# Kernel optimization log

Measured on AMD Instinct MI355X. Metric: run time of the kernel, lower is better.

The kernel has to match this reference:

```python
import jax, jax.numpy as jnp
import numpy as np

N_NODES = 50000
N_EDGES = 600000
F_IN, HID, N_CLS = 128, 128, 40
NEG_SLOPE = 0.2


def _gat_conv(x, src, dst, W, a_src, a_dst, b, num_nodes):
    # x: [N, Fin] -> h: [N, H]  (heads=1 PyG GATConv)
    h = x @ W
    s_src = h @ a_src  # [N]
    s_dst = h @ a_dst  # [N]
    e = jax.nn.leaky_relu(s_src[src] + s_dst[dst], NEG_SLOPE)  # [E]
    # numerically-stable softmax over incoming edges per destination node
    m = jax.ops.segment_max(e, dst, num_segments=num_nodes)  # [N]
    ex = jnp.exp(e - m[dst])
    denom = jax.ops.segment_sum(ex, dst, num_segments=num_nodes)  # [N]
    alpha = ex / denom[dst]  # [E]
    out = jax.ops.segment_sum(alpha[:, None] * h[src], dst, num_segments=num_nodes)
    return out + b


def setup_inputs() -> dict:
    key = jax.random.key(0)
    ks = jax.random.split(key, 10)
    x = jax.random.normal(ks[0], (N_NODES, F_IN), dtype=jnp.float32)
    edge_index = jax.random.randint(ks[1], (2, N_EDGES), 0, N_NODES, dtype=jnp.int64)
    sd = lambda fin: 1.0 / np.sqrt(fin)
    return {
        "x": x,
        "edge_index": edge_index,
        "W1": jax.random.normal(ks[2], (F_IN, HID), dtype=jnp.float32) * sd(F_IN),
        "a1_src": jax.random.normal(ks[3], (HID,), dtype=jnp.float32) * sd(HID),
        "a1_dst": jax.random.normal(ks[4], (HID,), dtype=jnp.float32) * sd(HID),
        "b1": jnp.zeros((HID,), dtype=jnp.float32),
        "W2": jax.random.normal(ks[5], (HID, HID), dtype=jnp.float32) * sd(HID),
        "a2_src": jax.random.normal(ks[6], (HID,), dtype=jnp.float32) * sd(HID),
        "a2_dst": jax.random.normal(ks[7], (HID,), dtype=jnp.float32) * sd(HID),
        "b2": jnp.zeros((HID,), dtype=jnp.float32),
        "Wl": jax.random.normal(ks[8], (HID, N_CLS), dtype=jnp.float32) * sd(HID),
        "bl": jnp.zeros((N_CLS,), dtype=jnp.float32),
    }


def reference(x, edge_index, W1, a1_src, a1_dst, b1, W2, a2_src, a2_dst, b2, Wl, bl):
    n = x.shape[0]
    # PyG GATConv adds self loops by default
    loops = jnp.arange(n, dtype=edge_index.dtype)
    src = jnp.concatenate([edge_index[0], loops])
    dst = jnp.concatenate([edge_index[1], loops])
    h = jax.nn.relu(_gat_conv(x, src, dst, W1, a1_src, a1_dst, b1, n))
    # F.dropout(training=self.training): eval mode -> identity
    h = _gat_conv(h, src, dst, W2, a2_src, a2_dst, b2, n)
    logits = jax.nn.log_softmax(h @ Wl + bl, axis=1)
    return (logits, edge_index)
```

## Files before the change

kernel.cpp:

```cpp
#include <hip/hip_runtime.h>
#include <hip/hip_bf16.h>
#include <math.h>

#define N_NODES 50000
#define N_EDGES 600000
#define TOT_E   (N_EDGES + N_NODES)
#define FDIM    128
#define HROW    64
#define NCLS    40
#define SCAN_B  1024

__device__ inline float bf16_lo(uint32_t u) { return __uint_as_float(u << 16); }
__device__ inline float bf16_hi(uint32_t u) { return __uint_as_float(u & 0xffff0000u); }
__device__ inline uint32_t bf16_pack(float a, float b) {
    uint32_t ua = __float_as_uint(a), ub = __float_as_uint(b);
    uint32_t ra = (ua + 0x7fffu + ((ua >> 16) & 1u)) >> 16;
    uint32_t rb = (ub + 0x7fffu + ((ub >> 16) & 1u)) >> 16;
    return ra | (rb << 16);
}

__global__ void init_counts(int* __restrict__ counts) {
    int i = blockIdx.x * blockDim.x + threadIdx.x;
    if (i < N_NODES) counts[i] = 1;
}

__global__ void hist_kernel(const int* __restrict__ ei, int* __restrict__ counts) {
    int i = blockIdx.x * blockDim.x + threadIdx.x;
    if (i >= N_EDGES / 4) return;
    int4 d = ((const int4*)(ei + N_EDGES))[i];
    atomicAdd(&counts[d.x], 1);
    atomicAdd(&counts[d.y], 1);
    atomicAdd(&counts[d.z], 1);
    atomicAdd(&counts[d.w], 1);
}

__global__ void scan1_kernel(const int* __restrict__ counts, int* __restrict__ excl,
                             int* __restrict__ bsums, int n) {
    __shared__ int ws[16];
    int gid = blockIdx.x * SCAN_B + threadIdx.x;
    int wv = threadIdx.x >> 6, lane = threadIdx.x & 63;
    int v = (gid < n) ? counts[gid] : 0;
    int incl = v;
    #pragma unroll
    for (int off = 1; off < 64; off <<= 1) {
        int t = __shfl_up(incl, off, 64);
        if (lane >= off) incl += t;
    }
    if (lane == 63) ws[wv] = incl;
    __syncthreads();
    int woff = 0;
    for (int i = 0; i < wv; i++) woff += ws[i];
    if (gid < n) excl[gid] = woff + incl - v;
    if (threadIdx.x == SCAN_B - 1) bsums[blockIdx.x] = woff + incl;
}

__global__ void scan3_kernel(int* __restrict__ rowptr, const int* __restrict__ bsums,
                             int* __restrict__ cursor, int n, int total) {
    __shared__ int base_s;
    if (threadIdx.x < 64) {
        int v = (threadIdx.x < (int)blockIdx.x) ? bsums[threadIdx.x] : 0;
        #pragma unroll
        for (int off = 32; off > 0; off >>= 1) v += __shfl_down(v, off, 64);
        if (threadIdx.x == 0) base_s = v;
    }
    __syncthreads();
    int base = base_s;
    int gid = blockIdx.x * SCAN_B + threadIdx.x;
    if (gid < n) {
        int v = rowptr[gid] + base;
        rowptr[gid] = v;
        cursor[gid] = v;
    }
    if (gid == 0) rowptr[n] = total;
}

#define SCAT_T ((N_EDGES / 4) + N_NODES)
__global__ void scatter_kernel(const int* __restrict__ ei, int* __restrict__ cursor,
                               int* __restrict__ adj) {
    int i = blockIdx.x * blockDim.x + threadIdx.x;
    if (i >= SCAT_T) return;
    if (i < N_EDGES / 4) {
        int4 s4 = ((const int4*)ei)[i];
        int4 d4 = ((const int4*)(ei + N_EDGES))[i];
        adj[atomicAdd(&cursor[d4.x], 1)] = s4.x;
        adj[atomicAdd(&cursor[d4.y], 1)] = s4.y;
        adj[atomicAdd(&cursor[d4.z], 1)] = s4.z;
        adj[atomicAdd(&cursor[d4.w], 1)] = s4.w;
    } else {
        int nd = i - N_EDGES / 4;
        adj[atomicAdd(&cursor[nd], 1)] = nd;
    }
}

__global__ void prep_wa(const float* __restrict__ W1, const float* __restrict__ a1s,
                        const float* __restrict__ a1d, const float* __restrict__ W2,
                        const float* __restrict__ a2s, const float* __restrict__ a2d,
                        float* __restrict__ wa) {
    int t = threadIdx.x;
    int vec = t >> 7, k = t & 127;
    const float* W = (vec < 2) ? W1 : W2;
    const float* a = (vec == 0) ? a1s : (vec == 1) ? a1d : (vec == 2) ? a2s : a2d;
    float s = 0.f;
    #pragma unroll 4
    for (int j = 0; j < FDIM; j += 4) {
        float4 wv = *(const float4*)&W[k * FDIM + j];
        float4 av = *(const float4*)&a[j];
        s += wv.x * av.x + wv.y * av.y + wv.z * av.z + wv.w * av.w;
    }
    wa[vec * FDIM + k] = s;
}

#define GR 16
template <bool BF16IN>
__global__ __launch_bounds__(128) void gemm_att_kernel(
        const void* __restrict__ Xin, const float* __restrict__ W,
        const float* __restrict__ wa_s, const float* __restrict__ wa_d,
        uint32_t* __restrict__ H, float* __restrict__ ssrc, float* __restrict__ sdst) {
    __shared__ float xs[GR][FDIM];
    int tid  = threadIdx.x;
    int row0 = blockIdx.x * GR;

    if (BF16IN) {
        const uint32_t* Xp = (const uint32_t*)Xin + (size_t)row0 * HROW;
        #pragma unroll
        for (int i = 0; i < 8; i++) {
            int idx = tid + 128 * i;
            uint32_t u = Xp[idx];
            int r = idx >> 6, cc = idx & 63;
            xs[r][2 * cc]     = bf16_lo(u);
            xs[r][2 * cc + 1] = bf16_hi(u);
        }
    } else {
        const float4* Xv = (const float4*)((const float*)Xin + (size_t)row0 * FDIM);
        float4* xsv = (float4*)&xs[0][0];
        #pragma unroll
        for (int i = 0; i < 4; i++) xsv[tid + 128 * i] = Xv[tid + 128 * i];
    }
    __syncthreads();

    int c  = tid & 63;
    int rh = (tid >> 6) * 8;

    float2 acc[8];
    #pragma unroll
    for (int r = 0; r < 8; r++) acc[r] = make_float2(0.f, 0.f);

    #pragma unroll 2
    for (int k = 0; k < FDIM; k += 4) {
        float2 w01[4];
        #pragma unroll
        for (int kk = 0; kk < 4; kk++)
            w01[kk] = *(const float2*)&W[(k + kk) * FDIM + 2 * c];
        #pragma unroll
        for (int r = 0; r < 8; r++) {
            float4 xv = *(const float4*)&xs[rh + r][k];
            acc[r].x += xv.x * w01[0].x + xv.y * w01[1].x + xv.z * w01[2].x + xv.w * w01[3].x;
            acc[r].y += xv.x * w01[0].y + xv.y * w01[1].y + xv.z * w01[2].y + xv.w * w01[3].y;
        }
    }
    #pragma unroll
    for (int r = 0; r < 8; r++)
        H[(size_t)(row0 + rh + r) * HROW + c] = bf16_pack(acc[r].x, acc[r].y);

    int slot = tid >> 2, q = tid & 3;
    int r = slot >> 1;
    const float* av = (slot & 1) ? wa_d : wa_s;
    float p = 0.f;
    #pragma unroll
    for (int k = q * 32; k < q * 32 + 32; k += 4) {
        float4 xv = *(const float4*)&xs[r][k];
        p += xv.x * av[k] + xv.y * av[k + 1] + xv.z * av[k + 2] + xv.w * av[k + 3];
    }
    p += __shfl_down(p, 1, 4);
    p += __shfl_down(p, 2, 4);
    if (q == 0) { if (slot & 1) sdst[row0 + r] = p; else ssrc[row0 + r] = p; }
}

__global__ __launch_bounds__(128) void gat_aggregate(
        const uint32_t* __restrict__ h, const float* __restrict__ ssrc,
        const float* __restrict__ sdst, const int* __restrict__ rowptr,
        const int* __restrict__ adj, const float* __restrict__ bias,
        uint32_t* __restrict__ out, int do_relu) {
    int wv = threadIdx.x >> 6, lane = threadIdx.x & 63;
    int n = blockIdx.x * 2 + wv;
    __shared__ __align__(16) float wbuf[2][64];
    __shared__ __align__(16) int   sbuf[2][64];

    int beg = rowptr[n], deg = rowptr[n + 1] - beg;
    float sd = sdst[n];

    float ax0 = 0.f, ay0 = 0.f, ax1 = 0.f, ay1 = 0.f;
    float dsum = 0.f;

    for (int base = 0; base < deg; base += 64) {
        int c = min(64, deg - base);
        if (lane < c) {
            int s = adj[beg + base + lane];
            float e = ssrc[s] + sd;
            e = (e >= 0.f) ? e : 0.2f * e;
            float w = __expf(e);
            wbuf[wv][lane] = w;
            sbuf[wv][lane] = s;
            dsum += w;
        }
        asm volatile("s_waitcnt lgkmcnt(0)" ::: "memory");

        int j = 0;
        for (; j + 8 <= c; j += 8) {
            float4 wa4 = *(const float4*)&wbuf[wv][j];
            float4 wb4 = *(const float4*)&wbuf[wv][j + 4];
            int4   sa4 = *(const int4*)&sbuf[wv][j];
            int4   sb4 = *(const int4*)&sbuf[wv][j + 4];
            uint32_t u0 = h[(size_t)sa4.x * HROW + lane];
            uint32_t u1 = h[(size_t)sa4.y * HROW + lane];
            uint32_t u2 = h[(size_t)sa4.z * HROW + lane];
            uint32_t u3 = h[(size_t)sa4.w * HROW + lane];
            uint32_t u4 = h[(size_t)sb4.x * HROW + lane];
            uint32_t u5 = h[(size_t)sb4.y * HROW + lane];
            uint32_t u6 = h[(size_t)sb4.z * HROW + lane];
            uint32_t u7 = h[(size_t)sb4.w * HROW + lane];
            ax0 += wa4.x * bf16_lo(u0); ay0 += wa4.x * bf16_hi(u0);
            ax1 += wa4.y * bf16_lo(u1); ay1 += wa4.y * bf16_hi(u1);
            ax0 += wa4.z * bf16_lo(u2); ay0 += wa4.z * bf16_hi(u2);
            ax1 += wa4.w * bf16_lo(u3); ay1 += wa4.w * bf16_hi(u3);
            ax0 += wb4.x * bf16_lo(u4); ay0 += wb4.x * bf16_hi(u4);
            ax1 += wb4.y * bf16_lo(u5); ay1 += wb4.y * bf16_hi(u5);
            ax0 += wb4.z * bf16_lo(u6); ay0 += wb4.z * bf16_hi(u6);
            ax1 += wb4.w * bf16_lo(u7); ay1 += wb4.w * bf16_hi(u7);
        }
        for (; j + 4 <= c; j += 4) {
            float4 w4 = *(const float4*)&wbuf[wv][j];
            int4   s4 = *(const int4*)&sbuf[wv][j];
            uint32_t u0 = h[(size_t)s4.x * HROW + lane];
            uint32_t u1 = h[(size_t)s4.y * HROW + lane];
            uint32_t u2 = h[(size_t)s4.z * HROW + lane];
            uint32_t u3 = h[(size_t)s4.w * HROW + lane];
            ax0 += w4.x * bf16_lo(u0); ay0 += w4.x * bf16_hi(u0);
            ax1 += w4.y * bf16_lo(u1); ay1 += w4.y * bf16_hi(u1);
            ax0 += w4.z * bf16_lo(u2); ay0 += w4.z * bf16_hi(u2);
            ax1 += w4.w * bf16_lo(u3); ay1 += w4.w * bf16_hi(u3);
        }
        for (; j < c; j++) {
            float w = wbuf[wv][j];
            int   s = sbuf[wv][j];
            uint32_t u = h[(size_t)s * HROW + lane];
            ax0 += w * bf16_lo(u); ay0 += w * bf16_hi(u);
        }
        asm volatile("" ::: "memory");
    }

    #pragma unroll
    for (int off = 32; off > 0; off >>= 1) dsum += __shfl_xor(dsum, off, 64);
    float inv = 1.f / dsum;
    float2 b2 = ((const float2*)bias)[lane];
    float vx = (ax0 + ax1) * inv + b2.x;
    float vy = (ay0 + ay1) * inv + b2.y;
    if (do_relu) { vx = fmaxf(vx, 0.f); vy = fmaxf(vy, 0.f); }
    out[(size_t)n * HROW + lane] = bf16_pack(vx, vy);
}

__global__ __launch_bounds__(128) void classifier_kernel(
        const uint32_t* __restrict__ H, const float* __restrict__ Wl,
        const float* __restrict__ bl, float* __restrict__ out) {
    __shared__ float xs[16][FDIM];
    int tid  = threadIdx.x;
    int row0 = blockIdx.x * 16;
    const uint32_t* Hp = H + (size_t)row0 * HROW;
    #pragma unroll
    for (int i = 0; i < 8; i++) {
        int idx = tid + 128 * i;
        uint32_t u = Hp[idx];
        int r = idx >> 6, cc = idx & 63;
        xs[r][2 * cc]     = bf16_lo(u);
        xs[r][2 * cc + 1] = bf16_hi(u);
    }
    __syncthreads();

    int c = tid & 63, hw = tid >> 6;
    float acc[8];
    float blc = (c < NCLS) ? bl[c] : 0.f;
    #pragma unroll
    for (int r = 0; r < 8; r++) acc[r] = blc;

    #pragma unroll 2
    for (int k = 0; k < FDIM; k += 4) {
        float w0 = 0.f, w1 = 0.f, w2 = 0.f, w3 = 0.f;
        if (c < NCLS) {
            w0 = Wl[(k + 0) * NCLS + c]; w1 = Wl[(k + 1) * NCLS + c];
            w2 = Wl[(k + 2) * NCLS + c]; w3 = Wl[(k + 3) * NCLS + c];
        }
        #pragma unroll
        for (int r = 0; r < 8; r++) {
            float4 xv = *(const float4*)&xs[hw * 8 + r][k];
            acc[r] += xv.x * w0 + xv.y * w1 + xv.z * w2 + xv.w * w3;
        }
    }
    #pragma unroll
    for (int r = 0; r < 8; r++) {
        float v = (c < NCLS) ? acc[r] : -INFINITY;
        float mx = v;
        #pragma unroll
        for (int off = 32; off > 0; off >>= 1) mx = fmaxf(mx, __shfl_xor(mx, off, 64));
        float ex = (c < NCLS) ? expf(v - mx) : 0.f;
        #pragma unroll
        for (int off = 32; off > 0; off >>= 1) ex += __shfl_xor(ex, off, 64);
        float ls = logf(ex);
        if (c < NCLS) out[(size_t)(row0 + hw * 8 + r) * NCLS + c] = v - mx - ls;
    }
}

__global__ void edge_copy_kernel(const int* __restrict__ ei, float* __restrict__ out) {
    int i = blockIdx.x * blockDim.x + threadIdx.x;
    if (i >= (2 * N_EDGES) / 4) return;
    int4 v = ((const int4*)ei)[i];
    ((float4*)out)[i] = make_float4((float)v.x, (float)v.y, (float)v.z, (float)v.w);
}

extern "C" void kernel_launch(void* const* d_in, const int* in_sizes, int n_in,
                              void* d_out, int out_size, void* d_ws, size_t ws_size,
                              hipStream_t stream) {
    const float* x   = (const float*)d_in[0];
    const int*   ei  = (const int*)d_in[1];
    const float* W1  = (const float*)d_in[2];
    const float* a1s = (const float*)d_in[3];
    const float* a1d = (const float*)d_in[4];
    const float* b1  = (const float*)d_in[5];
    const float* W2  = (const float*)d_in[6];
    const float* a2s = (const float*)d_in[7];
    const float* a2d = (const float*)d_in[8];
    const float* b2  = (const float*)d_in[9];
    const float* Wl  = (const float*)d_in[10];
    const float* bl  = (const float*)d_in[11];
    float* out = (float*)d_out;

    char* ws = (char*)d_ws;
    size_t off = 0;
    auto alloc = [&](size_t bytes) {
        void* p = ws + off;
        off = (off + bytes + 255) & ~(size_t)255;
        return p;
    };
    int*      row_ptr = (int*)alloc((N_NODES + 1) * sizeof(int));
    int*      cursor  = (int*)alloc(N_NODES * sizeof(int));
    int*      counts  = (int*)alloc(N_NODES * sizeof(int));
    int*      bsums   = (int*)alloc(64 * sizeof(int));
    int*      adj     = (int*)alloc(TOT_E * sizeof(int));
    uint32_t* hA      = (uint32_t*)alloc((size_t)N_NODES * HROW * sizeof(uint32_t));
    uint32_t* hB      = (uint32_t*)alloc((size_t)N_NODES * HROW * sizeof(uint32_t));
    float*    ssrc    = (float*)alloc(N_NODES * sizeof(float));
    float*    sdst    = (float*)alloc(N_NODES * sizeof(float));
    float*    wa      = (float*)alloc(4 * FDIM * sizeof(float));

    hipLaunchKernelGGL(prep_wa, dim3(1), dim3(512), 0, stream, W1, a1s, a1d, W2, a2s, a2d, wa);

    hipLaunchKernelGGL(init_counts, dim3((N_NODES + 255) / 256), dim3(256), 0, stream, counts);
    hipLaunchKernelGGL(hist_kernel, dim3((N_EDGES / 4 + 255) / 256), dim3(256), 0, stream, ei, counts);
    int nscan = (N_NODES + SCAN_B - 1) / SCAN_B;
    hipLaunchKernelGGL(scan1_kernel, dim3(nscan), dim3(SCAN_B), 0, stream, counts, row_ptr, bsums, N_NODES);
    hipLaunchKernelGGL(scan3_kernel, dim3(nscan), dim3(SCAN_B), 0, stream, row_ptr, bsums, cursor, N_NODES, TOT_E);
    hipLaunchKernelGGL(scatter_kernel, dim3((SCAT_T + 255) / 256), dim3(256), 0, stream, ei, cursor, adj);

    hipLaunchKernelGGL((gemm_att_kernel<false>), dim3(N_NODES / GR), dim3(128), 0, stream,
                       (const void*)x, W1, wa + 0, wa + FDIM, hA, ssrc, sdst);
    hipLaunchKernelGGL(gat_aggregate, dim3(N_NODES / 2), dim3(128), 0, stream,
                       hA, ssrc, sdst, row_ptr, adj, b1, hB, 1);

    hipLaunchKernelGGL((gemm_att_kernel<true>), dim3(N_NODES / GR), dim3(128), 0, stream,
                       (const void*)hB, W2, wa + 2 * FDIM, wa + 3 * FDIM, hA, ssrc, sdst);
    hipLaunchKernelGGL(gat_aggregate, dim3(N_NODES / 2), dim3(128), 0, stream,
                       hA, ssrc, sdst, row_ptr, adj, b2, hB, 0);

    hipLaunchKernelGGL(classifier_kernel, dim3(N_NODES / 16), dim3(128), 0, stream, hB, Wl, bl, out);
    hipLaunchKernelGGL(edge_copy_kernel, dim3(((2 * N_EDGES) / 4 + 255) / 256), dim3(256), 0, stream,
                       ei, out + (size_t)N_NODES * NCLS);
}
```

Baseline: 333.3 us.

## Replace scalar GEMM with bf16 MFMA kernel and split attention-score computation

Replaces the fp32 shared-memory FMA GEMM with a bf16 MFMA 16x16x32 kernel. Weights are pre-packed into per-lane fragment layout and x is pre-packed to bf16. The attention scores are now computed by a separate wave-per-node reduction kernel that reads the input features. This is meant to cut GEMM compute time using matrix cores, at the cost of extra kernel launches, an x packing pass, and bf16 rounding of the layer-1 input.

```diff
diff --git a/kernel.cpp b/kernel.cpp
--- a/kernel.cpp
+++ b/kernel.cpp
@@ -9,6 +9,10 @@
 #define HROW    64
 #define NCLS    40
 #define SCAN_B  1024
+
+typedef __attribute__((ext_vector_type(4))) float  f32x4;
+typedef __attribute__((ext_vector_type(8))) __bf16 bf16x8;
+union FragU { uint32_t u[4]; bf16x8 v; };
 
 __device__ inline float bf16_lo(uint32_t u) { return __uint_as_float(u << 16); }
 __device__ inline float bf16_hi(uint32_t u) { return __uint_as_float(u & 0xffff0000u); }
@@ -110,70 +114,99 @@
     wa[vec * FDIM + k] = s;
 }
 
-#define GR 16
+__global__ void pack_x(const float* __restrict__ x, uint32_t* __restrict__ Xp) {
+    int i = blockIdx.x * blockDim.x + threadIdx.x;
+    if (i >= N_NODES * HROW) return;
+    float2 v = ((const float2*)x)[i];
+    Xp[i] = bf16_pack(v.x, v.y);
+}
+
+__global__ void prep_wfrag(const float* __restrict__ W1, const float* __restrict__ W2,
+                           uint32_t* __restrict__ wf1, uint32_t* __restrict__ wf2) {
+    int t = blockIdx.x * blockDim.x + threadIdx.x;
+    if (t >= 4096) return;
+    const float* W = (t < 2048) ? W1 : W2;
+    uint32_t*   wf = (t < 2048) ? wf1 : wf2;
+    int q = t & 2047;
+    int lane = q & 63, nt = (q >> 6) & 7, kt = q >> 9;
+    int n = nt * 16 + (lane & 15), g = lane >> 4;
+    uint32_t frag[4];
+    #pragma unroll
+    for (int d = 0; d < 4; d++) {
+        int kb = kt * 32 + 4 * g + (d & 1) * 2 + (d >> 1) * 16;
+        frag[d] = bf16_pack(W[kb * FDIM + n], W[(kb + 1) * FDIM + n]);
+    }
+    ((uint4*)wf)[(kt * 8 + nt) * 64 + lane] = *(uint4*)frag;
+}
+
+__global__ __launch_bounds__(256) void mfma_gemm(
+        const uint32_t* __restrict__ Xp, const uint32_t* __restrict__ wf,
+        uint32_t* __restrict__ H) {
+    int lane = threadIdx.x & 63, wv = threadIdx.x >> 6;
+    int row0 = blockIdx.x * 64 + wv * 16;
+    if (row0 >= N_NODES) return;
+    int r = lane & 15, g = lane >> 4;
+
+    const uint32_t* xrow = Xp + (size_t)(row0 + r) * HROW + 2 * g;
+    FragU af[4];
+    #pragma unroll
+    for (int kt = 0; kt < 4; kt++) {
+        uint2 lo = *(const uint2*)(xrow + kt * 16);
+        uint2 hi = *(const uint2*)(xrow + kt * 16 + 8);
+        af[kt].u[0] = lo.x; af[kt].u[1] = lo.y;
+        af[kt].u[2] = hi.x; af[kt].u[3] = hi.y;
+    }
+
+    f32x4 acc[8] = {};
+    #pragma unroll
+    for (int kt = 0; kt < 4; kt++) {
+        #pragma unroll
+        for (int nt = 0; nt < 8; nt++) {
+            FragU bfr;
+            *(uint4*)bfr.u = ((const uint4*)wf)[(kt * 8 + nt) * 64 + lane];
+            acc[nt] = __builtin_amdgcn_mfma_f32_16x16x32_bf16(af[kt].v, bfr.v, acc[nt], 0, 0, 0);
+        }
+    }
+
+    #pragma unroll
+    for (int nt = 0; nt < 8; nt++) {
+        #pragma unroll
+        for (int j = 0; j < 4; j++) {
+            float v0 = acc[nt][j];
+            float v1 = __shfl_xor(v0, 1, 64);
+            if (!(r & 1)) {
+                uint32_t p = bf16_pack(v0, v1);
+                H[(size_t)(row0 + 4 * g + j) * HROW + nt * 8 + (r >> 1)] = p;
+            }
+        }
+    }
+}
+
 template <bool BF16IN>
-__global__ __launch_bounds__(128) void gemm_att_kernel(
-        const void* __restrict__ Xin, const float* __restrict__ W,
-        const float* __restrict__ wa_s, const float* __restrict__ wa_d,
-        uint32_t* __restrict__ H, float* __restrict__ ssrc, float* __restrict__ sdst) {
-    __shared__ float xs[GR][FDIM];
-    int tid  = threadIdx.x;
-    int row0 = blockIdx.x * GR;
-
+__global__ __launch_bounds__(256) void score_kernel(
+        const void* __restrict__ Xin, const float* __restrict__ wa_s,
+        const float* __restrict__ wa_d, float* __restrict__ ssrc,
+        float* __restrict__ sdst) {
+    int wv = threadIdx.x >> 6, lane = threadIdx.x & 63;
+    int n = blockIdx.x * 4 + wv;
+    float lo, hi;
     if (BF16IN) {
-        const uint32_t* Xp = (const uint32_t*)Xin + (size_t)row0 * HROW;
-        #pragma unroll
-        for (int i = 0; i < 8; i++) {
-            int idx = tid + 128 * i;
-            uint32_t u = Xp[idx];
-            int r = idx >> 6, cc = idx & 63;
-            xs[r][2 * cc]     = bf16_lo(u);
-            xs[r][2 * cc + 1] = bf16_hi(u);
-        }
+        uint32_t u = ((const uint32_t*)Xin)[(size_t)n * HROW + lane];
+        lo = bf16_lo(u); hi = bf16_hi(u);
     } else {
-        const float4* Xv = (const float4*)((const float*)Xin + (size_t)row0 * FDIM);
-        float4* xsv = (float4*)&xs[0][0];
-        #pragma unroll
-        for (int i = 0; i < 4; i++) xsv[tid + 128 * i] = Xv[tid + 128 * i];
-    }
-    __syncthreads();
-
-    int c  = tid & 63;
-    int rh = (tid >> 6) * 8;
-
-    float2 acc[8];
-    #pragma unroll
-    for (int r = 0; r < 8; r++) acc[r] = make_float2(0.f, 0.f);
-
-    #pragma unroll 2
-    for (int k = 0; k < FDIM; k += 4) {
-        float2 w01[4];
-        #pragma unroll
-        for (int kk = 0; kk < 4; kk++)
-            w01[kk] = *(const float2*)&W[(k + kk) * FDIM + 2 * c];
-        #pragma unroll
-        for (int r = 0; r < 8; r++) {
-            float4 xv = *(const float4*)&xs[rh + r][k];
-            acc[r].x += xv.x * w01[0].x + xv.y * w01[1].x + xv.z * w01[2].x + xv.w * w01[3].x;
-            acc[r].y += xv.x * w01[0].y + xv.y * w01[1].y + xv.z * w01[2].y + xv.w * w01[3].y;
-        }
-    }
-    #pragma unroll
-    for (int r = 0; r < 8; r++)
-        H[(size_t)(row0 + rh + r) * HROW + c] = bf16_pack(acc[r].x, acc[r].y);
-
-    int slot = tid >> 2, q = tid & 3;
-    int r = slot >> 1;
-    const float* av = (slot & 1) ? wa_d : wa_s;
-    float p = 0.f;
-    #pragma unroll
-    for (int k = q * 32; k < q * 32 + 32; k += 4) {
-        float4 xv = *(const float4*)&xs[r][k];
-        p += xv.x * av[k] + xv.y * av[k + 1] + xv.z * av[k + 2] + xv.w * av[k + 3];
-    }
-    p += __shfl_down(p, 1, 4);
-    p += __shfl_down(p, 2, 4);
-    if (q == 0) { if (slot & 1) sdst[row0 + r] = p; else ssrc[row0 + r] = p; }
+        float2 xv = ((const float2*)Xin)[(size_t)n * (FDIM / 2) + lane];
+        lo = xv.x; hi = xv.y;
+    }
+    float2 as = *(const float2*)&wa_s[2 * lane];
+    float2 ad = *(const float2*)&wa_d[2 * lane];
+    float s1 = lo * as.x + hi * as.y;
+    float s2 = lo * ad.x + hi * ad.y;
+    #pragma unroll
+    for (int off = 32; off > 0; off >>= 1) {
+        s1 += __shfl_xor(s1, off, 64);
+        s2 += __shfl_xor(s2, off, 64);
+    }
+    if (lane == 0) { ssrc[n] = s1; sdst[n] = s2; }
 }
 
 __global__ __launch_bounds__(128) void gat_aggregate(
@@ -345,13 +378,19 @@
     int*      counts  = (int*)alloc(N_NODES * sizeof(int));
     int*      bsums   = (int*)alloc(64 * sizeof(int));
     int*      adj     = (int*)alloc(TOT_E * sizeof(int));
+    uint32_t* Xp      = (uint32_t*)alloc((size_t)N_NODES * HROW * sizeof(uint32_t));
     uint32_t* hA      = (uint32_t*)alloc((size_t)N_NODES * HROW * sizeof(uint32_t));
     uint32_t* hB      = (uint32_t*)alloc((size_t)N_NODES * HROW * sizeof(uint32_t));
     float*    ssrc    = (float*)alloc(N_NODES * sizeof(float));
     float*    sdst    = (float*)alloc(N_NODES * sizeof(float));
     float*    wa      = (float*)alloc(4 * FDIM * sizeof(float));
+    uint32_t* wf1     = (uint32_t*)alloc(2048 * 4 * sizeof(uint32_t));
+    uint32_t* wf2     = (uint32_t*)alloc(2048 * 4 * sizeof(uint32_t));
+    uint32_t* hC      = Xp;
 
     hipLaunchKernelGGL(prep_wa, dim3(1), dim3(512), 0, stream, W1, a1s, a1d, W2, a2s, a2d, wa);
+    hipLaunchKernelGGL(pack_x, dim3((N_NODES * HROW) / 256), dim3(256), 0, stream, x, Xp);
+    hipLaunchKernelGGL(prep_wfrag, dim3(16), dim3(256), 0, stream, W1, W2, wf1, wf2);
 
     hipLaunchKernelGGL(init_counts, dim3((N_NODES + 255) / 256), dim3(256), 0, stream, counts);
     hipLaunchKernelGGL(hist_kernel, dim3((N_EDGES / 4 + 255) / 256), dim3(256), 0, stream, ei, counts);
@@ -360,17 +399,19 @@
     hipLaunchKernelGGL(scan3_kernel, dim3(nscan), dim3(SCAN_B), 0, stream, row_ptr, bsums, cursor, N_NODES, TOT_E);
     hipLaunchKernelGGL(scatter_kernel, dim3((SCAT_T + 255) / 256), dim3(256), 0, stream, ei, cursor, adj);
 
-    hipLaunchKernelGGL((gemm_att_kernel<false>), dim3(N_NODES / GR), dim3(128), 0, stream,
-                       (const void*)x, W1, wa + 0, wa + FDIM, hA, ssrc, sdst);
+    hipLaunchKernelGGL((score_kernel<false>), dim3(N_NODES / 4), dim3(256), 0, stream,
+                       (const void*)x, wa + 0, wa + FDIM, ssrc, sdst);
+    hipLaunchKernelGGL(mfma_gemm, dim3((N_NODES + 63) / 64), dim3(256), 0, stream, Xp, wf1, hA);
     hipLaunchKernelGGL(gat_aggregate, dim3(N_NODES / 2), dim3(128), 0, stream,
                        hA, ssrc, sdst, row_ptr, adj, b1, hB, 1);
 
-    hipLaunchKernelGGL((gemm_att_kernel<true>), dim3(N_NODES / GR), dim3(128), 0, stream,
-                       (const void*)hB, W2, wa + 2 * FDIM, wa + 3 * FDIM, hA, ssrc, sdst);
+    hipLaunchKernelGGL((score_kernel<true>), dim3(N_NODES / 4), dim3(256), 0, stream,
+                       (const void*)hB, wa + 2 * FDIM, wa + 3 * FDIM, ssrc, sdst);
+    hipLaunchKernelGGL(mfma_gemm, dim3((N_NODES + 63) / 64), dim3(256), 0, stream, hB, wf2, hA);
     hipLaunchKernelGGL(gat_aggregate, dim3(N_NODES / 2), dim3(128), 0, stream,
-                       hA, ssrc, sdst, row_ptr, adj, b2, hB, 0);
-
-    hipLaunchKernelGGL(classifier_kernel, dim3(N_NODES / 16), dim3(128), 0, stream, hB, Wl, bl, out);
+                       hA, ssrc, sdst, row_ptr, adj, b2, hC, 0);
+
+    hipLaunchKernelGGL(classifier_kernel, dim3(N_NODES / 16), dim3(128), 0, stream, hC, Wl, bl, out);
     hipLaunchKernelGGL(edge_copy_kernel, dim3(((2 * N_EDGES) / 4 + 255) / 256), dim3(256), 0, stream,
                        ei, out + (size_t)N_NODES * NCLS);
 }
```

Result: faster. 311.6 us (-6.5%).
